# Performance work log

Hardware: AMD Instinct MI355X
Metric: run time of the kernel (lower is better)

## Reference

```python
import jax, jax.numpy as jnp
import numpy as np

NUM_EXPERTS = 8
TOP_K = 2
HIDDEN = 1024
INTER = 2048
BATCH, SEQ = 2, 2048


def setup_inputs() -> dict:
    key = jax.random.key(0)
    k1, k2, k3, k4 = jax.random.split(key, 4)
    hidden_states = jax.random.normal(k1, (BATCH, SEQ, HIDDEN), dtype=jnp.float32)
    # 0.02 init scale keeps router softmax unsaturated and activations sane
    router_w = jax.random.normal(k2, (NUM_EXPERTS, HIDDEN), dtype=jnp.float32) * 0.02
    up_w = jax.random.normal(k3, (NUM_EXPERTS, HIDDEN, INTER), dtype=jnp.float32) * 0.02
    down_w = jax.random.normal(k4, (NUM_EXPERTS, INTER, HIDDEN), dtype=jnp.float32) * 0.02
    return {"hidden_states": hidden_states, "router_w": router_w, "up_w": up_w, "down_w": down_w}


def reference(hidden_states, router_w, up_w, down_w):
    batch, seq_len, hidden = hidden_states.shape
    flat = hidden_states.reshape(-1, hidden)            # [N, H]
    num_tokens = flat.shape[0]

    router_logits = flat @ router_w.T                   # [N, E]
    router_probs = jax.nn.softmax(router_logits, axis=-1)
    top_weights, top_indices = jax.lax.top_k(router_probs, TOP_K)  # [N, k]
    top_weights = top_weights / jnp.sum(top_weights, axis=-1, keepdims=True)

    # scatter normalized top-k weights into a dense [N, E] mask
    rows = jnp.arange(num_tokens)[:, None]
    expert_mask = jnp.zeros((num_tokens, NUM_EXPERTS), dtype=flat.dtype)
    expert_mask = expert_mask.at[rows, top_indices].set(top_weights)

    # dense path: all experts on all tokens via batched matmul
    h = jnp.einsum('nh,ehf->enf', flat, up_w)           # [E, N, F]
    h = jax.nn.gelu(h, approximate=False)               # torch nn.GELU default = erf
    expert_out = jnp.einsum('enf,efh->enh', h, down_w)  # [E, N, H]
    output = jnp.einsum('enh,ne->nh', expert_out, expert_mask)
    output = output.reshape(batch, seq_len, hidden)

    # load-balancing aux loss; f is computed under no_grad in torch
    one_hot = jnp.zeros((num_tokens, NUM_EXPERTS), dtype=jnp.float32)
    one_hot = one_hot.at[rows, top_indices].set(1.0)
    f = jax.lax.stop_gradient(jnp.sum(one_hot, axis=0) / (num_tokens * TOP_K))
    P = jnp.mean(router_probs, axis=0)
    aux_loss = NUM_EXPERTS * jnp.sum(f * P)
    return output, aux_loss
```

## Files before the change

### kernel.cpp

```cpp
#include <hip/hip_runtime.h>
#include <math.h>

#define NE 8
#define HD 1024
#define FD 2048
#define NT 4096
#define NSLOT (NT * 2)

typedef __attribute__((ext_vector_type(8))) _Float16 half8;
typedef __attribute__((ext_vector_type(4))) float floatx4;

__device__ __forceinline__ void gload_lds(const _Float16* g, _Float16* l) {
  __builtin_amdgcn_global_load_lds(
      (const __attribute__((address_space(1))) unsigned int*)g,
      (__attribute__((address_space(3))) unsigned int*)l, 16, 0, 0);
}

__global__ void cvt_x_kernel(const float* __restrict__ x, _Float16* __restrict__ xh) {
  size_t i = (size_t)(blockIdx.x * 256 + threadIdx.x) * 8;
  float4 f0 = *(const float4*)(x + i);
  float4 f1 = *(const float4*)(x + i + 4);
  union { _Float16 h[8]; uint4 v; } u;
  u.h[0] = (_Float16)f0.x; u.h[1] = (_Float16)f0.y;
  u.h[2] = (_Float16)f0.z; u.h[3] = (_Float16)f0.w;
  u.h[4] = (_Float16)f1.x; u.h[5] = (_Float16)f1.y;
  u.h[6] = (_Float16)f1.z; u.h[7] = (_Float16)f1.w;
  *(uint4*)(xh + i) = u.v;
}

__global__ void transpose_cvt(const float* __restrict__ in, _Float16* __restrict__ outp,
                              int R, int C) {
  __shared__ float t[32][33];
  int e = blockIdx.z;
  int r0 = blockIdx.x * 32, c0 = blockIdx.y * 32;
  int tx = threadIdx.x, ty = threadIdx.y;
  const float* src = in + (size_t)e * R * C;
#pragma unroll
  for (int i = 0; i < 4; i++)
    t[ty + 8 * i][tx] = src[(size_t)(r0 + ty + 8 * i) * C + c0 + tx];
  __syncthreads();
  _Float16* dst = outp + (size_t)e * R * C;
  int tid = ty * 32 + tx;
  int cl = tid >> 3, rq = tid & 7;
  union { _Float16 h[4]; uint2 v; } o;
#pragma unroll
  for (int k = 0; k < 4; k++) o.h[k] = (_Float16)t[rq * 4 + k][cl];
  *(uint2*)(dst + (size_t)(c0 + cl) * R + r0 + rq * 4) = o.v;
}

__global__ __launch_bounds__(256) void router_probs_kernel(
    const float* __restrict__ x, const float* __restrict__ rw,
    float* __restrict__ probs, int* __restrict__ sel_e, float* __restrict__ sel_w) {
  int n = blockIdx.x * 4 + (threadIdx.x >> 6);
  int lane = threadIdx.x & 63;
  const float* xr = x + (size_t)n * HD;
  float xv[16];
#pragma unroll
  for (int t = 0; t < 16; t++) xv[t] = xr[lane + 64 * t];
  float logits[NE];
#pragma unroll
  for (int e = 0; e < NE; e++) {
    const float* w = rw + (size_t)e * HD;
    float acc = 0.f;
#pragma unroll
    for (int t = 0; t < 16; t++) acc += xv[t] * w[lane + 64 * t];
    for (int off = 32; off > 0; off >>= 1) acc += __shfl_down(acc, off);
    logits[e] = acc;
  }
  if (lane == 0) {
    float mx = logits[0];
#pragma unroll
    for (int e = 1; e < NE; e++) mx = fmaxf(mx, logits[e]);
    float p[NE]; float s = 0.f;
#pragma unroll
    for (int e = 0; e < NE; e++) { p[e] = expf(logits[e] - mx); s += p[e]; }
    float inv = 1.f / s;
#pragma unroll
    for (int e = 0; e < NE; e++) { p[e] *= inv; probs[n * NE + e] = p[e]; }
    int i1 = 0;
#pragma unroll
    for (int e = 1; e < NE; e++) if (p[e] > p[i1]) i1 = e;
    int i2 = -1; float p2 = -1.f;
#pragma unroll
    for (int e = 0; e < NE; e++) {
      if (e == i1) continue;
      if (p[e] > p2) { p2 = p[e]; i2 = e; }
    }
    float wn = 1.f / (p[i1] + p[i2]);
    sel_e[n * 2 + 0] = i1; sel_w[n * 2 + 0] = p[i1] * wn;
    sel_e[n * 2 + 1] = i2; sel_w[n * 2 + 1] = p[i2] * wn;
  }
}

__global__ __launch_bounds__(1024) void router_reduce_kernel(
    const float* __restrict__ probs, const int* __restrict__ sel_e,
    int* __restrict__ counts, int* __restrict__ offs, int* __restrict__ cursor,
    float* __restrict__ aux_out) {
  int t = threadIdx.x;
  int lane = t & 63, wave = t >> 6;
  float ps[NE];
  int cn[NE];
#pragma unroll
  for (int e = 0; e < NE; e++) { ps[e] = 0.f; cn[e] = 0; }
  for (int r = t; r < NT; r += 1024) {
    const float* pr = probs + (size_t)r * NE;
#pragma unroll
    for (int e = 0; e < NE; e++) ps[e] += pr[e];
  }
  for (int i = t; i < NSLOT; i += 1024) {
    int e = sel_e[i];
#pragma unroll
    for (int j = 0; j < NE; j++) cn[j] += (e == j) ? 1 : 0;
  }
  for (int off = 32; off > 0; off >>= 1) {
#pragma unroll
    for (int e = 0; e < NE; e++) {
      ps[e] += __shfl_down(ps[e], off);
      cn[e] += __shfl_down(cn[e], off);
    }
  }
  __shared__ float sps[16][NE];
  __shared__ int scn[16][NE];
  if (lane == 0) {
#pragma unroll
    for (int e = 0; e < NE; e++) { sps[wave][e] = ps[e]; scn[wave][e] = cn[e]; }
  }
  __syncthreads();
  if (t == 0) {
    float tot_p[NE]; int tot_c[NE];
#pragma unroll
    for (int e = 0; e < NE; e++) { tot_p[e] = 0.f; tot_c[e] = 0; }
    for (int w = 0; w < 16; w++)
#pragma unroll
      for (int e = 0; e < NE; e++) { tot_p[e] += sps[w][e]; tot_c[e] += scn[w][e]; }
    int o = 0;
    float aux = 0.f;
    for (int e = 0; e < NE; e++) {
      counts[e] = tot_c[e];
      offs[e] = o; o += tot_c[e];
      cursor[e] = 0;
      aux += ((float)tot_c[e] / (float)NSLOT) * (tot_p[e] / (float)NT);
    }
    aux_out[0] = (float)NE * aux;
  }
}

__global__ __launch_bounds__(256) void build_gather(
    const int* __restrict__ sel_e, const float* __restrict__ sel_w,
    const int* __restrict__ offs, int* __restrict__ cursor,
    int* __restrict__ gtok, float* __restrict__ gw, int* __restrict__ srow) {
  __shared__ int lh[NE], lbase[NE];
  int t = threadIdx.x;
  int i = blockIdx.x * 256 + t;
  if (t < NE) lh[t] = 0;
  __syncthreads();
  int e = sel_e[i];
  int lrank = atomicAdd(&lh[e], 1);
  __syncthreads();
  if (t < NE) lbase[t] = atomicAdd(&cursor[t], lh[t]);
  __syncthreads();
  int row = offs[e] + lbase[e] + lrank;
  gtok[row] = i >> 1;
  gw[row] = sel_w[i];
  srow[i] = row;
}

template <int KDIM, int NDIM, bool IS_UP>
__global__ __launch_bounds__(256, 3) void moe_gemm2(
    const _Float16* __restrict__ Abase, const _Float16* __restrict__ Bt,
    const int* __restrict__ counts, const int* __restrict__ offs,
    const int* __restrict__ gtok, const float* __restrict__ gw,
    _Float16* __restrict__ Hout, float* __restrict__ Dout) {
  int e = blockIdx.x;
  int cnt = counts[e];
  int m0 = blockIdx.y * 128;
  if (m0 >= cnt) return;
  int n0 = blockIdx.z * 128;
  int off = offs[e];

  __shared__ __align__(16) _Float16 As[128 * 64];
  __shared__ __align__(16) _Float16 Bs[128 * 64];

  int tid = threadIdx.x;
  int lane = tid & 63, wave = tid >> 6;
  int wm = (wave >> 1) * 64, wn = (wave & 1) * 64;

  int srow8 = lane >> 3;
  int chunk = (lane & 7) ^ srow8;
  const _Float16* ga[4];
  const _Float16* gb[4];
  _Float16* lA[4];
  _Float16* lB[4];
#pragma unroll
  for (int j = 0; j < 4; j++) {
    int r = wave * 32 + j * 8 + srow8;
    int am = m0 + r;
    if (am > cnt - 1) am = cnt - 1;
    if (IS_UP) {
      ga[j] = Abase + (size_t)gtok[off + am] * KDIM + chunk * 8;
    } else {
      ga[j] = Abase + (size_t)(off + am) * KDIM + chunk * 8;
    }
    gb[j] = Bt + ((size_t)e * NDIM + n0 + r) * KDIM + chunk * 8;
    lA[j] = As + (wave * 32 + j * 8) * 64;
    lB[j] = Bs + (wave * 32 + j * 8) * 64;
  }

  floatx4 acc[4][4];
#pragma unroll
  for (int i = 0; i < 4; i++)
#pragma unroll
    for (int j = 0; j < 4; j++) acc[i][j] = (floatx4){0.f, 0.f, 0.f, 0.f};

  int fr = lane & 15, g = lane >> 4;
  int sw0 = ((g) ^ (fr & 7)) * 8;
  int sw1 = ((4 + g) ^ (fr & 7)) * 8;

  for (int kt = 0; kt < KDIM / 64; kt++) {
    __syncthreads();
#pragma unroll
    for (int j = 0; j < 4; j++) gload_lds(ga[j], lA[j]);
#pragma unroll
    for (int j = 0; j < 4; j++) gload_lds(gb[j], lB[j]);
#pragma unroll
    for (int j = 0; j < 4; j++) { ga[j] += 64; gb[j] += 64; }
    __syncthreads();

    half8 af[4], bfv[4];
#pragma unroll
    for (int t = 0; t < 4; t++) {
      af[t] = *(const half8*)(As + (wm + t * 16 + fr) * 64 + sw0);
      bfv[t] = *(const half8*)(Bs + (wn + t * 16 + fr) * 64 + sw0);
    }
#pragma unroll
    for (int i = 0; i < 4; i++)
#pragma unroll
      for (int j = 0; j < 4; j++)
        acc[i][j] = __builtin_amdgcn_mfma_f32_16x16x32_f16(af[i], bfv[j], acc[i][j], 0, 0, 0);
#pragma unroll
    for (int t = 0; t < 4; t++) {
      af[t] = *(const half8*)(As + (wm + t * 16 + fr) * 64 + sw1);
      bfv[t] = *(const half8*)(Bs + (wn + t * 16 + fr) * 64 + sw1);
    }
#pragma unroll
    for (int i = 0; i < 4; i++)
#pragma unroll
      for (int j = 0; j < 4; j++)
        acc[i][j] = __builtin_amdgcn_mfma_f32_16x16x32_f16(af[i], bfv[j], acc[i][j], 0, 0, 0);
  }

  int cq = (lane >> 4) * 4, cc = lane & 15;
#pragma unroll
  for (int i = 0; i < 4; i++) {
#pragma unroll
    for (int r = 0; r < 4; r++) {
      int m = wm + i * 16 + cq + r;
      if (m0 + m < cnt) {
        if (IS_UP) {
          float w = gw[off + m0 + m];
          _Float16* hrow = Hout + (size_t)(off + m0 + m) * NDIM + n0;
#pragma unroll
          for (int j = 0; j < 4; j++) {
            float v = acc[i][j][r];
            float gl = 0.5f * v * (1.f + erff(v * 0.70710678118f));
            hrow[wn + j * 16 + cc] = (_Float16)(gl * w);
          }
        } else {
          float* orow = Dout + (size_t)(off + m0 + m) * NDIM + n0;
#pragma unroll
          for (int j = 0; j < 4; j++) orow[wn + j * 16 + cc] = acc[i][j][r];
        }
      }
    }
  }
}

__global__ __launch_bounds__(256) void combine_kernel(
    const float* __restrict__ Dout, const int* __restrict__ srow,
    float* __restrict__ out) {
  int n = blockIdx.x;
  int t = threadIdx.x;
  int r0 = srow[n * 2], r1 = srow[n * 2 + 1];
  float4 a = *(const float4*)(Dout + (size_t)r0 * HD + t * 4);
  float4 b = *(const float4*)(Dout + (size_t)r1 * HD + t * 4);
  float4 c; c.x = a.x + b.x; c.y = a.y + b.y; c.z = a.z + b.z; c.w = a.w + b.w;
  *(float4*)(out + (size_t)n * HD + t * 4) = c;
}

extern "C" void kernel_launch(void* const* d_in, const int* in_sizes, int n_in,
                              void* d_out, int out_size, void* d_ws, size_t ws_size,
                              hipStream_t stream) {
  const float* x = (const float*)d_in[0];
  const float* rw = (const float*)d_in[1];
  const float* up_w = (const float*)d_in[2];
  const float* dn_w = (const float*)d_in[3];
  float* out = (float*)d_out;

  char* ws = (char*)d_ws;
  _Float16* Xh   = (_Float16*)(ws + 0);
  _Float16* Wut  = (_Float16*)(ws + 8388608);
  float*    Dout = (float*)(ws + 0);
  _Float16* Wdt  = (_Float16*)(ws + 41943040);
  _Float16* Hbuf = (_Float16*)(ws + 75497472);
  char* tail = ws + 109051904;
  int*   gtok   = (int*)(tail + 0);
  float* gw     = (float*)(tail + 32768);
  int*   sel_e  = (int*)(tail + 65536);
  float* sel_w  = (float*)(tail + 98304);
  int*   srow   = (int*)(tail + 131072);
  float* probs  = (float*)(tail + 163840);
  int*   counts = (int*)(tail + 294912);
  int*   offs   = (int*)(tail + 294944);
  int*   cursor = (int*)(tail + 294976);

  cvt_x_kernel<<<(NT * HD / 8) / 256, 256, 0, stream>>>(x, Xh);
  transpose_cvt<<<dim3(HD / 32, FD / 32, NE), dim3(32, 8), 0, stream>>>(up_w, Wut, HD, FD);
  transpose_cvt<<<dim3(FD / 32, HD / 32, NE), dim3(32, 8), 0, stream>>>(dn_w, Wdt, FD, HD);
  router_probs_kernel<<<NT / 4, 256, 0, stream>>>(x, rw, probs, sel_e, sel_w);
  router_reduce_kernel<<<1, 1024, 0, stream>>>(probs, sel_e, counts, offs, cursor,
                                               out + (size_t)NT * HD);
  build_gather<<<NSLOT / 256, 256, 0, stream>>>(sel_e, sel_w, offs, cursor, gtok, gw, srow);

  moe_gemm2<HD, FD, true><<<dim3(NE, 32, FD / 128), 256, 0, stream>>>(
      Xh, Wut, counts, offs, gtok, gw, Hbuf, nullptr);
  moe_gemm2<FD, HD, false><<<dim3(NE, 32, HD / 128), 256, 0, stream>>>(
      Hbuf, Wdt, counts, offs, gtok, gw, nullptr, Dout);
  combine_kernel<<<NT, 256, 0, stream>>>(Dout, srow, out);
}
```

Before: 314.3 us.

## Double-buffer MoE GEMM LDS tiles, fuse x conversion into router, widen transpose

The grouped GEMM now uses two LDS buffers per operand and issues the next K-tile's global-to-LDS loads before computing the current tile, with explicit waitcnt and barriers, so load latency overlaps MFMA work. Occupancy hint drops from 3 to 2 blocks per CU because LDS use doubles. The separate fp32-to-fp16 conversion kernel for x is removed and folded into the router kernel, which already reads x, saving one launch and one pass over x. The weight transpose-convert kernel now handles 32x64 tiles with 16-byte stores instead of 32x32 with 8-byte stores.

```diff
diff --git a/kernel.cpp b/kernel.cpp
--- a/kernel.cpp
+++ b/kernel.cpp
@@ -16,40 +16,28 @@
       (__attribute__((address_space(3))) unsigned int*)l, 16, 0, 0);
 }
 
-__global__ void cvt_x_kernel(const float* __restrict__ x, _Float16* __restrict__ xh) {
-  size_t i = (size_t)(blockIdx.x * 256 + threadIdx.x) * 8;
-  float4 f0 = *(const float4*)(x + i);
-  float4 f1 = *(const float4*)(x + i + 4);
-  union { _Float16 h[8]; uint4 v; } u;
-  u.h[0] = (_Float16)f0.x; u.h[1] = (_Float16)f0.y;
-  u.h[2] = (_Float16)f0.z; u.h[3] = (_Float16)f0.w;
-  u.h[4] = (_Float16)f1.x; u.h[5] = (_Float16)f1.y;
-  u.h[6] = (_Float16)f1.z; u.h[7] = (_Float16)f1.w;
-  *(uint4*)(xh + i) = u.v;
-}
-
 __global__ void transpose_cvt(const float* __restrict__ in, _Float16* __restrict__ outp,
                               int R, int C) {
-  __shared__ float t[32][33];
+  __shared__ float t[32][65];
   int e = blockIdx.z;
-  int r0 = blockIdx.x * 32, c0 = blockIdx.y * 32;
+  int r0 = blockIdx.x * 32, c0 = blockIdx.y * 64;
   int tx = threadIdx.x, ty = threadIdx.y;
   const float* src = in + (size_t)e * R * C;
 #pragma unroll
-  for (int i = 0; i < 4; i++)
-    t[ty + 8 * i][tx] = src[(size_t)(r0 + ty + 8 * i) * C + c0 + tx];
+  for (int i = 0; i < 8; i++)
+    t[ty + 4 * i][tx] = src[(size_t)(r0 + ty + 4 * i) * C + c0 + tx];
   __syncthreads();
   _Float16* dst = outp + (size_t)e * R * C;
-  int tid = ty * 32 + tx;
-  int cl = tid >> 3, rq = tid & 7;
-  union { _Float16 h[4]; uint2 v; } o;
-#pragma unroll
-  for (int k = 0; k < 4; k++) o.h[k] = (_Float16)t[rq * 4 + k][cl];
-  *(uint2*)(dst + (size_t)(c0 + cl) * R + r0 + rq * 4) = o.v;
+  int tid = ty * 64 + tx;
+  int col = tid >> 2, rq = tid & 3;
+  union { _Float16 h[8]; uint4 v; } o;
+#pragma unroll
+  for (int k = 0; k < 8; k++) o.h[k] = (_Float16)t[rq * 8 + k][col];
+  *(uint4*)(dst + (size_t)(c0 + col) * R + r0 + rq * 8) = o.v;
 }
 
 __global__ __launch_bounds__(256) void router_probs_kernel(
-    const float* __restrict__ x, const float* __restrict__ rw,
+    const float* __restrict__ x, const float* __restrict__ rw, _Float16* __restrict__ xh,
     float* __restrict__ probs, int* __restrict__ sel_e, float* __restrict__ sel_w) {
   int n = blockIdx.x * 4 + (threadIdx.x >> 6);
   int lane = threadIdx.x & 63;
@@ -57,6 +45,9 @@
   float xv[16];
 #pragma unroll
   for (int t = 0; t < 16; t++) xv[t] = xr[lane + 64 * t];
+  _Float16* xhr = xh + (size_t)n * HD;
+#pragma unroll
+  for (int t = 0; t < 16; t++) xhr[lane + 64 * t] = (_Float16)xv[t];
   float logits[NE];
 #pragma unroll
   for (int e = 0; e < NE; e++) {
@@ -166,7 +157,7 @@
 }
 
 template <int KDIM, int NDIM, bool IS_UP>
-__global__ __launch_bounds__(256, 3) void moe_gemm2(
+__global__ __launch_bounds__(256, 2) void moe_gemm2(
     const _Float16* __restrict__ Abase, const _Float16* __restrict__ Bt,
     const int* __restrict__ counts, const int* __restrict__ offs,
     const int* __restrict__ gtok, const float* __restrict__ gw,
@@ -178,8 +169,8 @@
   int n0 = blockIdx.z * 128;
   int off = offs[e];
 
-  __shared__ __align__(16) _Float16 As[128 * 64];
-  __shared__ __align__(16) _Float16 Bs[128 * 64];
+  __shared__ __align__(16) _Float16 As[2][128 * 64];
+  __shared__ __align__(16) _Float16 Bs[2][128 * 64];
 
   int tid = threadIdx.x;
   int lane = tid & 63, wave = tid >> 6;
@@ -189,8 +180,7 @@
   int chunk = (lane & 7) ^ srow8;
   const _Float16* ga[4];
   const _Float16* gb[4];
-  _Float16* lA[4];
-  _Float16* lB[4];
+  int sbase = wave * 32 * 64;
 #pragma unroll
   for (int j = 0; j < 4; j++) {
     int r = wave * 32 + j * 8 + srow8;
@@ -202,8 +192,6 @@
       ga[j] = Abase + (size_t)(off + am) * KDIM + chunk * 8;
     }
     gb[j] = Bt + ((size_t)e * NDIM + n0 + r) * KDIM + chunk * 8;
-    lA[j] = As + (wave * 32 + j * 8) * 64;
-    lB[j] = Bs + (wave * 32 + j * 8) * 64;
   }
 
   floatx4 acc[4][4];
@@ -216,21 +204,23 @@
   int sw0 = ((g) ^ (fr & 7)) * 8;
   int sw1 = ((4 + g) ^ (fr & 7)) * 8;
 
-  for (int kt = 0; kt < KDIM / 64; kt++) {
-    __syncthreads();
-#pragma unroll
-    for (int j = 0; j < 4; j++) gload_lds(ga[j], lA[j]);
-#pragma unroll
-    for (int j = 0; j < 4; j++) gload_lds(gb[j], lB[j]);
+  auto stage = [&](int buf) {
+#pragma unroll
+    for (int j = 0; j < 4; j++) gload_lds(ga[j], &As[buf][sbase + j * 512]);
+#pragma unroll
+    for (int j = 0; j < 4; j++) gload_lds(gb[j], &Bs[buf][sbase + j * 512]);
 #pragma unroll
     for (int j = 0; j < 4; j++) { ga[j] += 64; gb[j] += 64; }
-    __syncthreads();
-
+  };
+
+  auto compute = [&](int buf) {
+    const _Float16* Ab = &As[buf][0];
+    const _Float16* Bb = &Bs[buf][0];
     half8 af[4], bfv[4];
 #pragma unroll
     for (int t = 0; t < 4; t++) {
-      af[t] = *(const half8*)(As + (wm + t * 16 + fr) * 64 + sw0);
-      bfv[t] = *(const half8*)(Bs + (wn + t * 16 + fr) * 64 + sw0);
+      af[t] = *(const half8*)(Ab + (wm + t * 16 + fr) * 64 + sw0);
+      bfv[t] = *(const half8*)(Bb + (wn + t * 16 + fr) * 64 + sw0);
     }
 #pragma unroll
     for (int i = 0; i < 4; i++)
@@ -239,15 +229,30 @@
         acc[i][j] = __builtin_amdgcn_mfma_f32_16x16x32_f16(af[i], bfv[j], acc[i][j], 0, 0, 0);
 #pragma unroll
     for (int t = 0; t < 4; t++) {
-      af[t] = *(const half8*)(As + (wm + t * 16 + fr) * 64 + sw1);
-      bfv[t] = *(const half8*)(Bs + (wn + t * 16 + fr) * 64 + sw1);
+      af[t] = *(const half8*)(Ab + (wm + t * 16 + fr) * 64 + sw1);
+      bfv[t] = *(const half8*)(Bb + (wn + t * 16 + fr) * 64 + sw1);
     }
 #pragma unroll
     for (int i = 0; i < 4; i++)
 #pragma unroll
       for (int j = 0; j < 4; j++)
         acc[i][j] = __builtin_amdgcn_mfma_f32_16x16x32_f16(af[i], bfv[j], acc[i][j], 0, 0, 0);
-  }
+  };
+
+  constexpr int NK = KDIM / 64;
+  stage(0);
+  for (int kt = 0; kt < NK - 1; ++kt) {
+    int cur = kt & 1;
+    stage(cur ^ 1);
+    asm volatile("s_waitcnt vmcnt(8)" ::: "memory");
+    __builtin_amdgcn_s_barrier();
+    compute(cur);
+    asm volatile("s_waitcnt lgkmcnt(0)" ::: "memory");
+    __builtin_amdgcn_s_barrier();
+  }
+  asm volatile("s_waitcnt vmcnt(0)" ::: "memory");
+  __builtin_amdgcn_s_barrier();
+  compute((NK - 1) & 1);
 
   int cq = (lane >> 4) * 4, cc = lane & 15;
 #pragma unroll
@@ -266,7 +271,7 @@
             hrow[wn + j * 16 + cc] = (_Float16)(gl * w);
           }
         } else {
-          float* orow = Dout + (size_t)(off + m0 + m) * NDIM + n0;
+          float* orow = Dout + (size_t)(off + m0 + m) * HD + n0;
 #pragma unroll
           for (int j = 0; j < 4; j++) orow[wn + j * 16 + cc] = acc[i][j][r];
         }
@@ -313,10 +318,9 @@
   int*   offs   = (int*)(tail + 294944);
   int*   cursor = (int*)(tail + 294976);
 
-  cvt_x_kernel<<<(NT * HD / 8) / 256, 256, 0, stream>>>(x, Xh);
-  transpose_cvt<<<dim3(HD / 32, FD / 32, NE), dim3(32, 8), 0, stream>>>(up_w, Wut, HD, FD);
-  transpose_cvt<<<dim3(FD / 32, HD / 32, NE), dim3(32, 8), 0, stream>>>(dn_w, Wdt, FD, HD);
-  router_probs_kernel<<<NT / 4, 256, 0, stream>>>(x, rw, probs, sel_e, sel_w);
+  transpose_cvt<<<dim3(HD / 32, FD / 64, NE), dim3(64, 4), 0, stream>>>(up_w, Wut, HD, FD);
+  transpose_cvt<<<dim3(FD / 32, HD / 64, NE), dim3(64, 4), 0, stream>>>(dn_w, Wdt, FD, HD);
+  router_probs_kernel<<<NT / 4, 256, 0, stream>>>(x, rw, Xh, probs, sel_e, sel_w);
   router_reduce_kernel<<<1, 1024, 0, stream>>>(probs, sel_e, counts, offs, cursor,
                                                out + (size_t)NT * HD);
   build_gather<<<NSLOT / 256, 256, 0, stream>>>(sel_e, sel_w, offs, cursor, gtok, gw, srow);
```

Measured after the change: 349.3 us. 11.2% more time.

## Fuse x conversion into router, widen weight transpose, atomically combine down-proj output

Applied to the files above, without the earlier changes.

Folds the fp16 conversion of x into the router kernel so x is read once. Rewrites the weight transpose to use float4 loads and 16-byte stores over 32x128 tiles. Removes the separate combine kernel: the down-projection GEMM now atomically adds each expert's output straight into the zeroed output rows, which adds a memset and float atomic contention and makes the summation order nondeterministic.

```diff
diff --git a/kernel.cpp b/kernel.cpp
--- a/kernel.cpp
+++ b/kernel.cpp
@@ -16,40 +16,34 @@
       (__attribute__((address_space(3))) unsigned int*)l, 16, 0, 0);
 }
 
-__global__ void cvt_x_kernel(const float* __restrict__ x, _Float16* __restrict__ xh) {
-  size_t i = (size_t)(blockIdx.x * 256 + threadIdx.x) * 8;
-  float4 f0 = *(const float4*)(x + i);
-  float4 f1 = *(const float4*)(x + i + 4);
-  union { _Float16 h[8]; uint4 v; } u;
-  u.h[0] = (_Float16)f0.x; u.h[1] = (_Float16)f0.y;
-  u.h[2] = (_Float16)f0.z; u.h[3] = (_Float16)f0.w;
-  u.h[4] = (_Float16)f1.x; u.h[5] = (_Float16)f1.y;
-  u.h[6] = (_Float16)f1.z; u.h[7] = (_Float16)f1.w;
-  *(uint4*)(xh + i) = u.v;
-}
-
-__global__ void transpose_cvt(const float* __restrict__ in, _Float16* __restrict__ outp,
-                              int R, int C) {
-  __shared__ float t[32][33];
+__global__ __launch_bounds__(256) void transpose_cvt(const float* __restrict__ in,
+                                                     _Float16* __restrict__ outp,
+                                                     int R, int C) {
+  __shared__ float t[32][132];
   int e = blockIdx.z;
-  int r0 = blockIdx.x * 32, c0 = blockIdx.y * 32;
-  int tx = threadIdx.x, ty = threadIdx.y;
+  int r0 = blockIdx.x * 32, c0 = blockIdx.y * 128;
+  int tid = threadIdx.x;
+  int f4c = tid & 31, rr = tid >> 5;
   const float* src = in + (size_t)e * R * C;
 #pragma unroll
-  for (int i = 0; i < 4; i++)
-    t[ty + 8 * i][tx] = src[(size_t)(r0 + ty + 8 * i) * C + c0 + tx];
+  for (int i = 0; i < 4; i++) {
+    float4 v = *(const float4*)(src + (size_t)(r0 + rr + 8 * i) * C + c0 + f4c * 4);
+    *(float4*)&t[rr + 8 * i][f4c * 4] = v;
+  }
   __syncthreads();
   _Float16* dst = outp + (size_t)e * R * C;
-  int tid = ty * 32 + tx;
-  int cl = tid >> 3, rq = tid & 7;
-  union { _Float16 h[4]; uint2 v; } o;
-#pragma unroll
-  for (int k = 0; k < 4; k++) o.h[k] = (_Float16)t[rq * 4 + k][cl];
-  *(uint2*)(dst + (size_t)(c0 + cl) * R + r0 + rq * 4) = o.v;
+  int oc = tid >> 1, rh = (tid & 1) * 16;
+  union { _Float16 h[8]; uint4 v; } o;
+#pragma unroll
+  for (int k2 = 0; k2 < 2; k2++) {
+#pragma unroll
+    for (int k = 0; k < 8; k++) o.h[k] = (_Float16)t[rh + k2 * 8 + k][oc];
+    *(uint4*)(dst + (size_t)(c0 + oc) * R + r0 + rh + k2 * 8) = o.v;
+  }
 }
 
 __global__ __launch_bounds__(256) void router_probs_kernel(
-    const float* __restrict__ x, const float* __restrict__ rw,
+    const float* __restrict__ x, const float* __restrict__ rw, _Float16* __restrict__ xh,
     float* __restrict__ probs, int* __restrict__ sel_e, float* __restrict__ sel_w) {
   int n = blockIdx.x * 4 + (threadIdx.x >> 6);
   int lane = threadIdx.x & 63;
@@ -57,6 +51,9 @@
   float xv[16];
 #pragma unroll
   for (int t = 0; t < 16; t++) xv[t] = xr[lane + 64 * t];
+  _Float16* xhr = xh + (size_t)n * HD;
+#pragma unroll
+  for (int t = 0; t < 16; t++) xhr[lane + 64 * t] = (_Float16)xv[t];
   float logits[NE];
 #pragma unroll
   for (int e = 0; e < NE; e++) {
@@ -148,7 +145,7 @@
 __global__ __launch_bounds__(256) void build_gather(
     const int* __restrict__ sel_e, const float* __restrict__ sel_w,
     const int* __restrict__ offs, int* __restrict__ cursor,
-    int* __restrict__ gtok, float* __restrict__ gw, int* __restrict__ srow) {
+    int* __restrict__ gtok, float* __restrict__ gw) {
   __shared__ int lh[NE], lbase[NE];
   int t = threadIdx.x;
   int i = blockIdx.x * 256 + t;
@@ -162,7 +159,6 @@
   int row = offs[e] + lbase[e] + lrank;
   gtok[row] = i >> 1;
   gw[row] = sel_w[i];
-  srow[i] = row;
 }
 
 template <int KDIM, int NDIM, bool IS_UP>
@@ -170,7 +166,7 @@
     const _Float16* __restrict__ Abase, const _Float16* __restrict__ Bt,
     const int* __restrict__ counts, const int* __restrict__ offs,
     const int* __restrict__ gtok, const float* __restrict__ gw,
-    _Float16* __restrict__ Hout, float* __restrict__ Dout) {
+    _Float16* __restrict__ Hout, float* __restrict__ Oout) {
   int e = blockIdx.x;
   int cnt = counts[e];
   int m0 = blockIdx.y * 128;
@@ -266,25 +262,14 @@
             hrow[wn + j * 16 + cc] = (_Float16)(gl * w);
           }
         } else {
-          float* orow = Dout + (size_t)(off + m0 + m) * NDIM + n0;
-#pragma unroll
-          for (int j = 0; j < 4; j++) orow[wn + j * 16 + cc] = acc[i][j][r];
+          int token = gtok[off + m0 + m];
+          float* orow = Oout + (size_t)token * HD + n0;
+#pragma unroll
+          for (int j = 0; j < 4; j++) atomicAdd(&orow[wn + j * 16 + cc], acc[i][j][r]);
         }
       }
     }
   }
-}
-
-__global__ __launch_bounds__(256) void combine_kernel(
-    const float* __restrict__ Dout, const int* __restrict__ srow,
-    float* __restrict__ out) {
-  int n = blockIdx.x;
-  int t = threadIdx.x;
-  int r0 = srow[n * 2], r1 = srow[n * 2 + 1];
-  float4 a = *(const float4*)(Dout + (size_t)r0 * HD + t * 4);
-  float4 b = *(const float4*)(Dout + (size_t)r1 * HD + t * 4);
-  float4 c; c.x = a.x + b.x; c.y = a.y + b.y; c.z = a.z + b.z; c.w = a.w + b.w;
-  *(float4*)(out + (size_t)n * HD + t * 4) = c;
 }
 
 extern "C" void kernel_launch(void* const* d_in, const int* in_sizes, int n_in,
@@ -299,7 +284,6 @@
   char* ws = (char*)d_ws;
   _Float16* Xh   = (_Float16*)(ws + 0);
   _Float16* Wut  = (_Float16*)(ws + 8388608);
-  float*    Dout = (float*)(ws + 0);
   _Float16* Wdt  = (_Float16*)(ws + 41943040);
   _Float16* Hbuf = (_Float16*)(ws + 75497472);
   char* tail = ws + 109051904;
@@ -307,23 +291,22 @@
   float* gw     = (float*)(tail + 32768);
   int*   sel_e  = (int*)(tail + 65536);
   float* sel_w  = (float*)(tail + 98304);
-  int*   srow   = (int*)(tail + 131072);
-  float* probs  = (float*)(tail + 163840);
-  int*   counts = (int*)(tail + 294912);
-  int*   offs   = (int*)(tail + 294944);
-  int*   cursor = (int*)(tail + 294976);
-
-  cvt_x_kernel<<<(NT * HD / 8) / 256, 256, 0, stream>>>(x, Xh);
-  transpose_cvt<<<dim3(HD / 32, FD / 32, NE), dim3(32, 8), 0, stream>>>(up_w, Wut, HD, FD);
-  transpose_cvt<<<dim3(FD / 32, HD / 32, NE), dim3(32, 8), 0, stream>>>(dn_w, Wdt, FD, HD);
-  router_probs_kernel<<<NT / 4, 256, 0, stream>>>(x, rw, probs, sel_e, sel_w);
+  float* probs  = (float*)(tail + 131072);
+  int*   counts = (int*)(tail + 262144);
+  int*   offs   = (int*)(tail + 262176);
+  int*   cursor = (int*)(tail + 262208);
+
+  hipMemsetAsync(out, 0, (size_t)NT * HD * sizeof(float), stream);
+
+  transpose_cvt<<<dim3(HD / 32, FD / 128, NE), 256, 0, stream>>>(up_w, Wut, HD, FD);
+  transpose_cvt<<<dim3(FD / 32, HD / 128, NE), 256, 0, stream>>>(dn_w, Wdt, FD, HD);
+  router_probs_kernel<<<NT / 4, 256, 0, stream>>>(x, rw, Xh, probs, sel_e, sel_w);
   router_reduce_kernel<<<1, 1024, 0, stream>>>(probs, sel_e, counts, offs, cursor,
                                                out + (size_t)NT * HD);
-  build_gather<<<NSLOT / 256, 256, 0, stream>>>(sel_e, sel_w, offs, cursor, gtok, gw, srow);
+  build_gather<<<NSLOT / 256, 256, 0, stream>>>(sel_e, sel_w, offs, cursor, gtok, gw);
 
   moe_gemm2<HD, FD, true><<<dim3(NE, 32, FD / 128), 256, 0, stream>>>(
       Xh, Wut, counts, offs, gtok, gw, Hbuf, nullptr);
   moe_gemm2<FD, HD, false><<<dim3(NE, 32, HD / 128), 256, 0, stream>>>(
-      Hbuf, Wdt, counts, offs, gtok, gw, nullptr, Dout);
-  combine_kernel<<<NT, 256, 0, stream>>>(Dout, srow, out);
-}
+      Hbuf, Wdt, counts, offs, gtok, gw, nullptr, out);
+}
```

Result: slower. 333.9 us (+6.2%).
